# Optimization experiments

Hardware: AMD Instinct MI355X
Metric: run time of the kernel (lower is better)

## Reference

```python
import jax, jax.numpy as jnp
import numpy as np

N_NODES = 100000
N_EDGES = 1200000
F_IN, HID, LAT = 128, 64, 32
N_GRAPHS = 512
NEG_SLOPE = 0.2  # PyG GATConv default


def setup_inputs() -> dict:
    key = jax.random.key(0)
    ks = jax.random.split(key, 20)
    inp = {
        'x': jax.random.normal(ks[0], (N_NODES, F_IN), jnp.float32),
        'edge_index': jax.random.randint(ks[1], (2, N_EDGES), 0, N_NODES, jnp.int32),
        'batch': jnp.sort(jax.random.randint(ks[2], (N_NODES,), 0, N_GRAPHS, jnp.int32)),
    }
    # GAT layer params: W [in,out], a_src/a_dst [out], bias [out] (heads=1)
    dims = [(F_IN, HID), (HID, HID), (HID, HID)]
    for i, (din, dout) in enumerate(dims):
        s = 1.0 / np.sqrt(din)
        inp[f'W{i}'] = jax.random.uniform(ks[3 + 4 * i], (din, dout), jnp.float32, -s, s)
        inp[f'a_src{i}'] = jax.random.normal(ks[4 + 4 * i], (dout,), jnp.float32) * 0.1
        inp[f'a_dst{i}'] = jax.random.normal(ks[5 + 4 * i], (dout,), jnp.float32) * 0.1
        inp[f'b{i}'] = jnp.zeros((dout,), jnp.float32)
    s = 1.0 / np.sqrt(HID)
    inp['fc_W'] = jax.random.uniform(ks[15], (HID, LAT), jnp.float32, -s, s)
    inp['fc_b'] = jnp.zeros((LAT,), jnp.float32)
    return inp


def _gat_layer(x, src, dst, W, a_src, a_dst, b, n):
    h = x @ W                                   # [N, out]
    e = (h @ a_src)[src] + (h @ a_dst)[dst]     # [E+N] raw scores
    e = jnp.where(e > 0, e, NEG_SLOPE * e)      # LeakyReLU
    # segmented softmax over incoming edges of each dst (self-loops guarantee non-empty)
    m = jax.ops.segment_max(e, dst, num_segments=n)
    w = jnp.exp(e - m[dst])
    denom = jax.ops.segment_sum(w, dst, num_segments=n)
    alpha = w / denom[dst]
    out = jax.ops.segment_sum(h[src] * alpha[:, None], dst, num_segments=n)
    return out + b


def reference(x, edge_index, batch, W0, a_src0, a_dst0, b0, W1, a_src1, a_dst1, b1,
              W2, a_src2, a_dst2, b2, fc_W, fc_b):
    n = x.shape[0]
    loops = jnp.arange(n, dtype=edge_index.dtype)
    src = jnp.concatenate([edge_index[0], loops])  # add_self_loops=True
    dst = jnp.concatenate([edge_index[1], loops])
    for (W, a_s, a_d, b) in ((W0, a_src0, a_dst0, b0),
                             (W1, a_src1, a_dst1, b1),
                             (W2, a_src2, a_dst2, b2)):
        x = jax.nn.relu(_gat_layer(x, src, dst, W, a_s, a_d, b, n))
    # dropout is identity in eval mode
    sums = jax.ops.segment_sum(x, batch, num_segments=N_GRAPHS)
    cnt = jax.ops.segment_sum(jnp.ones((n,), x.dtype), batch, num_segments=N_GRAPHS)
    pooled = sums / jnp.maximum(cnt, 1.0)[:, None]  # global_mean_pool
    return pooled @ fc_W + fc_b
```

## Files before the change

### kernel.cpp

```cpp
#include <hip/hip_runtime.h>
#include <hip/hip_bf16.h>
#include <hip/hip_fp16.h>

#define NN 100000
#define NE 1200000
#define NG 512
#define NBK ((NN + 511) / 512)
#define CAP 8192
#define SBATCH 4096
#define EPB (SBATCH / 256)
#define SA_BLOCKS ((NE + SBATCH - 1) / SBATCH)
#define TILES ((NN + 63) / 64)

__global__ void k_binitF(int* gcur) {
    int b = blockIdx.x * blockDim.x + threadIdx.x;
    if (b < NBK) gcur[b] = b * CAP;
}

__device__ __forceinline__ void sortA_body(
    const int* __restrict__ srcA, const int* __restrict__ dstA, int e,
    int* gcur, uint2* __restrict__ ebuf, int bid, int* smemInt) {
    int* cnt = smemInt;
    int* base = smemInt + NBK;
    const int t = threadIdx.x;
    const int i0 = bid * SBATCH;
    for (int b = t; b < NBK; b += 256) cnt[b] = 0;
    __syncthreads();
#pragma unroll
    for (int k = 0; k < EPB; ++k) {
        int i = i0 + k * 256 + t;
        if (i < e) atomicAdd(&cnt[dstA[i] >> 9], 1);
    }
    __syncthreads();
    for (int b = t; b < NBK; b += 256) {
        int c = cnt[b];
        base[b] = c ? atomicAdd(&gcur[b], c) : 0;
        cnt[b] = 0;
    }
    __syncthreads();
#pragma unroll
    for (int k = 0; k < EPB; ++k) {
        int i = i0 + k * 256 + t;
        if (i < e) {
            int d = dstA[i], s = srcA[i];
            int b = d >> 9;
            int off = atomicAdd(&cnt[b], 1);
            int slot = base[b] + off;
            if (slot < (b + 1) * CAP)
                ebuf[slot] = make_uint2((unsigned)s, (unsigned)d);
        }
    }
}

__global__ __launch_bounds__(256) void k_hist2(
    const uint2* __restrict__ ebuf, const int* __restrict__ gcur,
    int* __restrict__ cnt, int n) {
    __shared__ int c512[512];
    const int b = blockIdx.x;
    const int d0 = b << 9;
    const int hi = min(n - d0, 512);
    for (int j = threadIdx.x; j < 512; j += 256) c512[j] = 0;
    __syncthreads();
    const int beg = b * CAP, end = gcur[b];
    for (int i = beg + threadIdx.x; i < end; i += 256)
        atomicAdd(&c512[(int)ebuf[i].y - d0], 1);
    __syncthreads();
    for (int j = threadIdx.x; j < hi; j += 256) cnt[d0 + j] = c512[j] + 1;
}

__global__ void k_scan1(const int* __restrict__ cnt, int n, int* ex, int* blkSum) {
    __shared__ int s[1024];
    int i = blockIdx.x * 1024 + threadIdx.x;
    int v = (i < n) ? cnt[i] : 0;
    s[threadIdx.x] = v;
    __syncthreads();
    for (int off = 1; off < 1024; off <<= 1) {
        int t = (threadIdx.x >= off) ? s[threadIdx.x - off] : 0;
        __syncthreads();
        s[threadIdx.x] += t;
        __syncthreads();
    }
    if (i < n) ex[i] = s[threadIdx.x] - v;
    if (threadIdx.x == 1023) blkSum[blockIdx.x] = s[1023];
}

__global__ void k_scan2(const int* __restrict__ blkSum, int nb, int* blkOff, int* totalOut) {
    __shared__ int s[128];
    int t = threadIdx.x;
    int v = (t < nb) ? blkSum[t] : 0;
    s[t] = v;
    __syncthreads();
    for (int off = 1; off < 128; off <<= 1) {
        int x = (t >= off) ? s[t - off] : 0;
        __syncthreads();
        s[t] += x;
        __syncthreads();
    }
    if (t < nb) blkOff[t] = s[t] - v;
    if (t == 127) *totalOut = s[127];
}

__global__ void k_scan3(int* row_ptr, const int* __restrict__ blkOff, int n) {
    int i = blockIdx.x * blockDim.x + threadIdx.x;
    if (i < n) row_ptr[i] += blkOff[i >> 10];
}

__global__ __launch_bounds__(512) void k_sortB2(
    const uint2* __restrict__ ebuf, const int* __restrict__ gcur,
    const int* __restrict__ row_ptr, int n, int* __restrict__ col) {
    __shared__ int cur[512];
    const int b = blockIdx.x;
    const int d0 = b << 9;
    const int hi = min(n - d0, 512);
    for (int j = threadIdx.x; j < hi; j += 512) {
        int rp = row_ptr[d0 + j];
        col[rp] = d0 + j;
        cur[j] = rp + 1;
    }
    __syncthreads();
    const int beg = b * CAP, end = gcur[b];
    for (int i = beg + threadIdx.x; i < end; i += 512) {
        uint2 r = ebuf[i];
        int pos = atomicAdd(&cur[(int)r.y - d0], 1);
        col[pos] = (int)r.x;
    }
}

#define XP 36
#define WP 68
#define SMEM_FLOATS (64 * XP + 32 * WP)

template <int K, bool HIN>
__device__ __forceinline__ void gemm_body(
    const float* __restrict__ Xf, const __half* __restrict__ Xh,
    const float* __restrict__ W,
    const float* __restrict__ a_src, const float* __restrict__ a_dst,
    __half* __restrict__ H, float* __restrict__ ssrc, float* __restrict__ sdst,
    int n, int tile, float* __restrict__ Xs, float* __restrict__ Ws) {
    constexpr int KC = 32;
    constexpr int NC = K / KC;
    const int tid = threadIdx.x;
    const int row0 = tile * 64;
    const int tx = tid & 15, ty = tid >> 4;
    float acc[4][4] = {};

    for (int c = 0; c < NC; ++c) {
        if (c) __syncthreads();
        for (int i = tid; i < KC * 16; i += 256) {
            int k = i >> 4, c4 = i & 15;
            float4 v = reinterpret_cast<const float4*>(W + (size_t)(c * KC + k) * 64)[c4];
            *reinterpret_cast<float4*>(&Ws[k * WP + c4 * 4]) = v;
        }
        for (int i = tid; i < 64 * 8; i += 256) {
            int r = i >> 3, c4 = i & 7;
            int row = row0 + r;
            float4 v = make_float4(0.f, 0.f, 0.f, 0.f);
            if (row < n) {
                if constexpr (HIN) {
                    float2 raw = reinterpret_cast<const float2*>(Xh + (size_t)row * K + c * KC)[c4];
                    const __half2* ph = reinterpret_cast<const __half2*>(&raw);
                    float2 lo = __half22float2(ph[0]), hi = __half22float2(ph[1]);
                    v = make_float4(lo.x, lo.y, hi.x, hi.y);
                } else {
                    v = reinterpret_cast<const float4*>(Xf + (size_t)row * K + c * KC)[c4];
                }
            }
            *reinterpret_cast<float4*>(&Xs[r * XP + c4 * 4]) = v;
        }
        __syncthreads();

        for (int k = 0; k < KC; k += 4) {
            float4 xv[4], wv[4];
#pragma unroll
            for (int r = 0; r < 4; ++r)
                xv[r] = *reinterpret_cast<const float4*>(&Xs[(ty * 4 + r) * XP + k]);
#pragma unroll
            for (int j = 0; j < 4; ++j)
                wv[j] = *reinterpret_cast<const float4*>(&Ws[(k + j) * WP + tx * 4]);
#pragma unroll
            for (int r = 0; r < 4; ++r) {
                const float* xp = reinterpret_cast<const float*>(&xv[r]);
#pragma unroll
                for (int j = 0; j < 4; ++j) {
                    const float* wp = reinterpret_cast<const float*>(&wv[j]);
#pragma unroll
                    for (int cc = 0; cc < 4; ++cc) acc[r][cc] += xp[j] * wp[cc];
                }
            }
        }
    }

    float4 av = reinterpret_cast<const float4*>(a_src)[tx];
    float4 dv = reinterpret_cast<const float4*>(a_dst)[tx];
#pragma unroll
    for (int r = 0; r < 4; ++r) {
        int row = row0 + ty * 4 + r;
        if (row < n) {
            float2 packed;
            *reinterpret_cast<__half2*>(&packed.x) = __floats2half2_rn(acc[r][0], acc[r][1]);
            *reinterpret_cast<__half2*>(&packed.y) = __floats2half2_rn(acc[r][2], acc[r][3]);
            reinterpret_cast<float2*>(H + (size_t)row * 64)[tx] = packed;
            float ps = acc[r][0] * av.x + acc[r][1] * av.y + acc[r][2] * av.z + acc[r][3] * av.w;
            float pd = acc[r][0] * dv.x + acc[r][1] * dv.y + acc[r][2] * dv.z + acc[r][3] * dv.w;
#pragma unroll
            for (int off = 1; off < 16; off <<= 1) {
                ps += __shfl_xor(ps, off);
                pd += __shfl_xor(pd, off);
            }
            if (tx == 0) {
                ssrc[row] = ps;
                sdst[row] = pd;
            }
        }
    }
}

__global__ __launch_bounds__(256) void k_g0sA(
    const int* __restrict__ srcA, const int* __restrict__ dstA,
    int* gcur, uint2* __restrict__ ebuf,
    const float* __restrict__ Xf, const float* __restrict__ W,
    const float* __restrict__ a_src, const float* __restrict__ a_dst,
    __half* __restrict__ H, float* __restrict__ ssrc, float* __restrict__ sdst, int n) {
    __shared__ float smem[SMEM_FLOATS];
    if (blockIdx.x < TILES) {
        gemm_body<128, false>(Xf, nullptr, W, a_src, a_dst, H, ssrc, sdst, n,
                              blockIdx.x, smem, smem + 64 * XP);
    } else {
        sortA_body(srcA, dstA, NE, gcur, ebuf, blockIdx.x - TILES,
                   reinterpret_cast<int*>(smem));
    }
}

template <int K, bool HIN>
__global__ __launch_bounds__(256) void k_gemm_att(
    const float* __restrict__ Xf, const __half* __restrict__ Xh,
    const float* __restrict__ W,
    const float* __restrict__ a_src, const float* __restrict__ a_dst,
    __half* __restrict__ H, float* __restrict__ ssrc, float* __restrict__ sdst, int n) {
    __shared__ float smem[SMEM_FLOATS];
    gemm_body<K, HIN>(Xf, Xh, W, a_src, a_dst, H, ssrc, sdst, n,
                      blockIdx.x, smem, smem + 64 * XP);
}

__global__ __launch_bounds__(256) void k_agg5(
    const float2* __restrict__ H2, const float* __restrict__ ssrc,
    const float* __restrict__ sdst, const int* __restrict__ row_ptr,
    const int* __restrict__ col, const float4* __restrict__ bias4,
    float2* __restrict__ Yh2, int n) {
    const int wave = threadIdx.x >> 6, lane = threadIdx.x & 63;
    const int hf = lane >> 5, hl = lane & 31;
    const int base = blockIdx.x * 8 + wave * 2;
    const int dst = base + hf;

    int beg = 0, end = 0;
    if (dst < n) { beg = row_ptr[dst]; end = row_ptr[dst + 1]; }
    int deg = end - beg;
    int dmax = max(deg, __shfl_xor(deg, 32));

    if (dmax <= 32) {
        float sd = (dst < n) ? sdst[dst] : 0.f;
        int s_l = 0;
        float e = -INFINITY;
        if (hl < deg) {
            s_l = col[beg + hl];
            e = ssrc[s_l] + sd;
            e = (e > 0.f) ? e : 0.2f * e;
        }
        float m = e;
#pragma unroll
        for (int off = 16; off; off >>= 1) m = fmaxf(m, __shfl_xor(m, off));
        float w_l = (hl < deg) ? __expf(e - m) : 0.f;
        float den = w_l;
#pragma unroll
        for (int off = 16; off; off >>= 1) den += __shfl_xor(den, off);

        const int grp = hl >> 4, fl = hl & 15;
        float4 acc = make_float4(0.f, 0.f, 0.f, 0.f);
        for (int jj = 0; jj < deg; jj += 8) {
            int j0 = jj + grp, j1 = jj + 2 + grp, j2 = jj + 4 + grp, j3 = jj + 6 + grp;
            int s0 = __shfl(s_l, hf * 32 + j0), s1 = __shfl(s_l, hf * 32 + j1);
            int s2 = __shfl(s_l, hf * 32 + j2), s3 = __shfl(s_l, hf * 32 + j3);
            float w0 = __shfl(w_l, hf * 32 + j0), w1 = __shfl(w_l, hf * 32 + j1);
            float w2 = __shfl(w_l, hf * 32 + j2), w3 = __shfl(w_l, hf * 32 + j3);
            if (j0 < deg) {
                float2 raw = H2[(size_t)s0 * 16 + fl];
                const __half2* ph = reinterpret_cast<const __half2*>(&raw);
                float2 lo = __half22float2(ph[0]), hi = __half22float2(ph[1]);
                acc.x += w0 * lo.x; acc.y += w0 * lo.y;
                acc.z += w0 * hi.x; acc.w += w0 * hi.y;
            }
            if (j1 < deg) {
                float2 raw = H2[(size_t)s1 * 16 + fl];
                const __half2* ph = reinterpret_cast<const __half2*>(&raw);
                float2 lo = __half22float2(ph[0]), hi = __half22float2(ph[1]);
                acc.x += w1 * lo.x; acc.y += w1 * lo.y;
                acc.z += w1 * hi.x; acc.w += w1 * hi.y;
            }
            if (j2 < deg) {
                float2 raw = H2[(size_t)s2 * 16 + fl];
                const __half2* ph = reinterpret_cast<const __half2*>(&raw);
                float2 lo = __half22float2(ph[0]), hi = __half22float2(ph[1]);
                acc.x += w2 * lo.x; acc.y += w2 * lo.y;
                acc.z += w2 * hi.x; acc.w += w2 * hi.y;
            }
            if (j3 < deg) {
                float2 raw = H2[(size_t)s3 * 16 + fl];
                const __half2* ph = reinterpret_cast<const __half2*>(&raw);
                float2 lo = __half22float2(ph[0]), hi = __half22float2(ph[1]);
                acc.x += w3 * lo.x; acc.y += w3 * lo.y;
                acc.z += w3 * hi.x; acc.w += w3 * hi.y;
            }
        }
        acc.x += __shfl_xor(acc.x, 16);
        acc.y += __shfl_xor(acc.y, 16);
        acc.z += __shfl_xor(acc.z, 16);
        acc.w += __shfl_xor(acc.w, 16);
        if (grp == 0 && dst < n) {
            float inv = 1.f / den;
            float4 b = bias4[fl];
            float ox = fmaxf(acc.x * inv + b.x, 0.f);
            float oy = fmaxf(acc.y * inv + b.y, 0.f);
            float oz = fmaxf(acc.z * inv + b.z, 0.f);
            float ow = fmaxf(acc.w * inv + b.w, 0.f);
            float2 packed;
            *reinterpret_cast<__half2*>(&packed.x) = __floats2half2_rn(ox, oy);
            *reinterpret_cast<__half2*>(&packed.y) = __floats2half2_rn(oz, ow);
            Yh2[(size_t)dst * 16 + fl] = packed;
        }
    } else {
        for (int h = 0; h < 2; ++h) {
            int d = base + h;
            if (d >= n) break;
            int bg = row_ptr[d], en = row_ptr[d + 1];
            float sdd = sdst[d];
            float m = -INFINITY, d2 = 0.f;
            for (int c = bg; c < en; c += 64) {
                int j = c + lane;
                float e = -INFINITY;
                if (j < en) {
                    e = ssrc[col[j]] + sdd;
                    e = (e > 0.f) ? e : 0.2f * e;
                }
                float cm = e;
#pragma unroll
                for (int off = 32; off; off >>= 1) cm = fmaxf(cm, __shfl_xor(cm, off));
                float nm = fmaxf(m, cm);
                float term = (j < en) ? __expf(e - nm) : 0.f;
#pragma unroll
                for (int off = 32; off; off >>= 1) term += __shfl_xor(term, off);
                d2 = d2 * __expf(m - nm) + term;
                m = nm;
            }
            const int g4 = lane >> 4, fl = lane & 15;
            float4 acc = make_float4(0.f, 0.f, 0.f, 0.f);
            for (int jj = 0; jj < en - bg; jj += 8) {
                int j0 = bg + jj + g4, j1 = bg + jj + 4 + g4;
                if (j0 < en) {
                    int s = col[j0];
                    float e = ssrc[s] + sdd;
                    e = (e > 0.f) ? e : 0.2f * e;
                    float wgt = __expf(e - m);
                    float2 raw = H2[(size_t)s * 16 + fl];
                    const __half2* ph = reinterpret_cast<const __half2*>(&raw);
                    float2 lo = __half22float2(ph[0]), hi = __half22float2(ph[1]);
                    acc.x += wgt * lo.x; acc.y += wgt * lo.y;
                    acc.z += wgt * hi.x; acc.w += wgt * hi.y;
                }
                if (j1 < en) {
                    int s = col[j1];
                    float e = ssrc[s] + sdd;
                    e = (e > 0.f) ? e : 0.2f * e;
                    float wgt = __expf(e - m);
                    float2 raw = H2[(size_t)s * 16 + fl];
                    const __half2* ph = reinterpret_cast<const __half2*>(&raw);
                    float2 lo = __half22float2(ph[0]), hi = __half22float2(ph[1]);
                    acc.x += wgt * lo.x; acc.y += wgt * lo.y;
                    acc.z += wgt * hi.x; acc.w += wgt * hi.y;
                }
            }
#pragma unroll
            for (int off = 16; off < 64; off <<= 1) {
                acc.x += __shfl_xor(acc.x, off);
                acc.y += __shfl_xor(acc.y, off);
                acc.z += __shfl_xor(acc.z, off);
                acc.w += __shfl_xor(acc.w, off);
            }
            if (g4 == 0) {
                float inv = 1.f / d2;
                float4 b = bias4[fl];
                float ox = fmaxf(acc.x * inv + b.x, 0.f);
                float oy = fmaxf(acc.y * inv + b.y, 0.f);
                float oz = fmaxf(acc.z * inv + b.z, 0.f);
                float ow = fmaxf(acc.w * inv + b.w, 0.f);
                float2 packed;
                *reinterpret_cast<__half2*>(&packed.x) = __floats2half2_rn(ox, oy);
                *reinterpret_cast<__half2*>(&packed.y) = __floats2half2_rn(oz, ow);
                Yh2[(size_t)d * 16 + fl] = packed;
            }
        }
    }
}

__global__ void k_gstart(const int* __restrict__ batch, int n, int* gs) {
    int g = blockIdx.x * blockDim.x + threadIdx.x;
    if (g > NG) return;
    int lo = 0, hi = n;
    while (lo < hi) {
        int mid = (lo + hi) >> 1;
        if (batch[mid] < g) lo = mid + 1; else hi = mid;
    }
    gs[g] = lo;
}

__global__ __launch_bounds__(256) void k_pool_fc(
    const float2* __restrict__ Yh2, const int* __restrict__ gs,
    const float* __restrict__ fcW, const float* __restrict__ fcb,
    float* __restrict__ out) {
    __shared__ float4 part[4][16];
    __shared__ float p[64];
    const int g = blockIdx.x, tid = threadIdx.x;
    const int wave = tid >> 6, lane = tid & 63;
    const int grp = lane >> 4, fl = lane & 15;
    const int b = gs[g], e = gs[g + 1];

    float4 acc = make_float4(0.f, 0.f, 0.f, 0.f);
    for (int r = b + wave * 4 + grp; r < e; r += 16) {
        float2 raw = Yh2[(size_t)r * 16 + fl];
        const __half2* ph = reinterpret_cast<const __half2*>(&raw);
        float2 lo = __half22float2(ph[0]), hi = __half22float2(ph[1]);
        acc.x += lo.x; acc.y += lo.y; acc.z += hi.x; acc.w += hi.y;
    }
#pragma unroll
    for (int off = 16; off < 64; off <<= 1) {
        acc.x += __shfl_xor(acc.x, off);
        acc.y += __shfl_xor(acc.y, off);
        acc.z += __shfl_xor(acc.z, off);
        acc.w += __shfl_xor(acc.w, off);
    }
    if (grp == 0) part[wave][fl] = acc;
    __syncthreads();
    if (tid < 16) {
        float4 s0 = part[0][tid], s1 = part[1][tid], s2 = part[2][tid], s3 = part[3][tid];
        float inv = 1.f / (float)((e - b) > 0 ? (e - b) : 1);
        p[tid * 4 + 0] = (s0.x + s1.x + s2.x + s3.x) * inv;
        p[tid * 4 + 1] = (s0.y + s1.y + s2.y + s3.y) * inv;
        p[tid * 4 + 2] = (s0.z + s1.z + s2.z + s3.z) * inv;
        p[tid * 4 + 3] = (s0.w + s1.w + s2.w + s3.w) * inv;
    }
    __syncthreads();
    if (tid < 32) {
        float accO = fcb[tid];
#pragma unroll
        for (int k = 0; k < 64; ++k) accO += p[k] * fcW[k * 32 + tid];
        out[g * 32 + tid] = accO;
    }
}

extern "C" void kernel_launch(void* const* d_in, const int* in_sizes, int n_in,
                              void* d_out, int out_size, void* d_ws, size_t ws_size,
                              hipStream_t stream) {
    const float* x = (const float*)d_in[0];
    const int* ei = (const int*)d_in[1];
    const int* batch = (const int*)d_in[2];
    const float* W0 = (const float*)d_in[3];
    const float* as0 = (const float*)d_in[4];
    const float* ad0 = (const float*)d_in[5];
    const float* b0 = (const float*)d_in[6];
    const float* W1 = (const float*)d_in[7];
    const float* as1 = (const float*)d_in[8];
    const float* ad1 = (const float*)d_in[9];
    const float* b1 = (const float*)d_in[10];
    const float* W2 = (const float*)d_in[11];
    const float* as2 = (const float*)d_in[12];
    const float* ad2 = (const float*)d_in[13];
    const float* b2 = (const float*)d_in[14];
    const float* fcW = (const float*)d_in[15];
    const float* fcb = (const float*)d_in[16];
    float* out = (float*)d_out;

    char* w = (char*)d_ws;
    auto alloc = [&](size_t bytes) {
        void* p = (void*)w;
        w += (bytes + 255) & ~(size_t)255;
        return p;
    };
    int* cnt = (int*)alloc((size_t)NN * 4);
    int* row_ptr = (int*)alloc((size_t)(NN + 1) * 4);
    int* blkSum = (int*)alloc(512);
    int* blkOff = (int*)alloc(512);
    int* gcur = (int*)alloc((size_t)NBK * 4);
    int* col = (int*)alloc((size_t)(NE + NN) * 4);
    int* gs = (int*)alloc((size_t)(NG + 1) * 4);
    uint2* ebuf = (uint2*)alloc((size_t)NBK * CAP * 8);
    __half* Ha = (__half*)alloc((size_t)NN * 64 * 2);
    __half* Hb = (__half*)alloc((size_t)NN * 64 * 2);
    __half* Y = (__half*)alloc((size_t)NN * 64 * 2);
    float* ssA = (float*)alloc((size_t)NN * 4);
    float* sdA = (float*)alloc((size_t)NN * 4);
    float* ssB = (float*)alloc((size_t)NN * 4);
    float* sdB = (float*)alloc((size_t)NN * 4);

    const int* srcA = ei;
    const int* dstA = ei + NE;

    k_binitF<<<1, 256, 0, stream>>>(gcur);
    k_g0sA<<<TILES + SA_BLOCKS, 256, 0, stream>>>(srcA, dstA, gcur, ebuf,
                                                  x, W0, as0, ad0, Ha, ssA, sdA, NN);
    k_hist2<<<NBK, 256, 0, stream>>>(ebuf, gcur, cnt, NN);
    const int nb = (NN + 1023) / 1024;
    k_scan1<<<nb, 1024, 0, stream>>>(cnt, NN, row_ptr, blkSum);
    k_scan2<<<1, 128, 0, stream>>>(blkSum, nb, blkOff, row_ptr + NN);
    k_scan3<<<(NN + 255) / 256, 256, 0, stream>>>(row_ptr, blkOff, NN);
    k_sortB2<<<NBK, 512, 0, stream>>>(ebuf, gcur, row_ptr, NN, col);
    k_gstart<<<3, 256, 0, stream>>>(batch, NN, gs);

    const int agg_grid = (NN + 7) / 8;

    k_agg5<<<agg_grid, 256, 0, stream>>>((const float2*)Ha, ssA, sdA, row_ptr, col,
                                         (const float4*)b0, (float2*)Hb, NN);
    k_gemm_att<64, true><<<TILES, 256, 0, stream>>>(nullptr, Hb, W1, as1, ad1,
                                                    Ha, ssB, sdB, NN);
    k_agg5<<<agg_grid, 256, 0, stream>>>((const float2*)Ha, ssB, sdB, row_ptr, col,
                                         (const float4*)b1, (float2*)Hb, NN);
    k_gemm_att<64, true><<<TILES, 256, 0, stream>>>(nullptr, Hb, W2, as2, ad2,
                                                    Ha, ssA, sdA, NN);
    k_agg5<<<agg_grid, 256, 0, stream>>>((const float2*)Ha, ssA, sdA, row_ptr, col,
                                         (const float4*)b2, (float2*)Y, NN);

    k_pool_fc<<<NG, 256, 0, stream>>>((const float2*)Y, gs, fcW, fcb, out);
}
```

Measured before the change: 248.1 us.

## Replace histogram plus three-pass scan with bucket-level prefix and in-block placement

The per-node histogram and three-kernel global scan are replaced by a single small kernel that scans per-bucket edge counts and computes the graph starts, followed by one kernel per bucket that histograms, scans locally, writes row_ptr and places edges. This cuts the CSR build from six launches to two and drops the cnt/blkSum round trips through global memory. The placement kernel now reads ebuf twice within one block. The fused first kernel also runs the sort blocks ahead of the GEMM tiles.

```diff
diff --git a/kernel.cpp b/kernel.cpp
--- a/kernel.cpp
+++ b/kernel.cpp
@@ -52,76 +52,77 @@
     }
 }
 
-__global__ __launch_bounds__(256) void k_hist2(
+__global__ __launch_bounds__(256) void k_bucketPfx(
+    const int* __restrict__ gcur, int* __restrict__ bstart, int* __restrict__ row_ptr,
+    const int* __restrict__ batch, int* __restrict__ gs, int n) {
+    if (blockIdx.x == 0) {
+        __shared__ int s[256];
+        const int t = threadIdx.x;
+        int v = 0;
+        if (t < NBK) {
+            int d0 = t << 9;
+            int hi = min(n - d0, 512);
+            int edges = min(gcur[t] - t * CAP, CAP);
+            v = edges + hi;
+        }
+        s[t] = v;
+        __syncthreads();
+        for (int off = 1; off < 256; off <<= 1) {
+            int x = (t >= off) ? s[t - off] : 0;
+            __syncthreads();
+            s[t] += x;
+            __syncthreads();
+        }
+        if (t < NBK) bstart[t] = s[t] - v;
+        if (t == NBK - 1) row_ptr[n] = s[t];
+    } else {
+        int g = (blockIdx.x - 1) * 256 + threadIdx.x;
+        if (g > NG) return;
+        int lo = 0, hi = n;
+        while (lo < hi) {
+            int mid = (lo + hi) >> 1;
+            if (batch[mid] < g) lo = mid + 1; else hi = mid;
+        }
+        gs[g] = lo;
+    }
+}
+
+__global__ __launch_bounds__(512) void k_place(
     const uint2* __restrict__ ebuf, const int* __restrict__ gcur,
-    int* __restrict__ cnt, int n) {
-    __shared__ int c512[512];
+    const int* __restrict__ bstart, int* __restrict__ row_ptr,
+    int* __restrict__ col, int n) {
+    __shared__ int cnt[512];
+    __shared__ int scn[512];
     const int b = blockIdx.x;
     const int d0 = b << 9;
     const int hi = min(n - d0, 512);
-    for (int j = threadIdx.x; j < 512; j += 256) c512[j] = 0;
-    __syncthreads();
-    const int beg = b * CAP, end = gcur[b];
-    for (int i = beg + threadIdx.x; i < end; i += 256)
-        atomicAdd(&c512[(int)ebuf[i].y - d0], 1);
-    __syncthreads();
-    for (int j = threadIdx.x; j < hi; j += 256) cnt[d0 + j] = c512[j] + 1;
-}
-
-__global__ void k_scan1(const int* __restrict__ cnt, int n, int* ex, int* blkSum) {
-    __shared__ int s[1024];
-    int i = blockIdx.x * 1024 + threadIdx.x;
-    int v = (i < n) ? cnt[i] : 0;
-    s[threadIdx.x] = v;
-    __syncthreads();
-    for (int off = 1; off < 1024; off <<= 1) {
-        int t = (threadIdx.x >= off) ? s[threadIdx.x - off] : 0;
+    const int t = threadIdx.x;
+    cnt[t] = (t < hi) ? 1 : 0;
+    __syncthreads();
+    const int beg = b * CAP;
+    const int end = min(gcur[b], beg + CAP);
+    for (int i = beg + t; i < end; i += 512)
+        atomicAdd(&cnt[(int)ebuf[i].y - d0], 1);
+    __syncthreads();
+    int v = cnt[t];
+    scn[t] = v;
+    __syncthreads();
+    for (int off = 1; off < 512; off <<= 1) {
+        int x = (t >= off) ? scn[t - off] : 0;
         __syncthreads();
-        s[threadIdx.x] += t;
+        scn[t] += x;
         __syncthreads();
     }
-    if (i < n) ex[i] = s[threadIdx.x] - v;
-    if (threadIdx.x == 1023) blkSum[blockIdx.x] = s[1023];
-}
-
-__global__ void k_scan2(const int* __restrict__ blkSum, int nb, int* blkOff, int* totalOut) {
-    __shared__ int s[128];
-    int t = threadIdx.x;
-    int v = (t < nb) ? blkSum[t] : 0;
-    s[t] = v;
-    __syncthreads();
-    for (int off = 1; off < 128; off <<= 1) {
-        int x = (t >= off) ? s[t - off] : 0;
-        __syncthreads();
-        s[t] += x;
-        __syncthreads();
-    }
-    if (t < nb) blkOff[t] = s[t] - v;
-    if (t == 127) *totalOut = s[127];
-}
-
-__global__ void k_scan3(int* row_ptr, const int* __restrict__ blkOff, int n) {
-    int i = blockIdx.x * blockDim.x + threadIdx.x;
-    if (i < n) row_ptr[i] += blkOff[i >> 10];
-}
-
-__global__ __launch_bounds__(512) void k_sortB2(
-    const uint2* __restrict__ ebuf, const int* __restrict__ gcur,
-    const int* __restrict__ row_ptr, int n, int* __restrict__ col) {
-    __shared__ int cur[512];
-    const int b = blockIdx.x;
-    const int d0 = b << 9;
-    const int hi = min(n - d0, 512);
-    for (int j = threadIdx.x; j < hi; j += 512) {
-        int rp = row_ptr[d0 + j];
-        col[rp] = d0 + j;
-        cur[j] = rp + 1;
-    }
-    __syncthreads();
-    const int beg = b * CAP, end = gcur[b];
-    for (int i = beg + threadIdx.x; i < end; i += 512) {
+    int rp = bstart[b] + scn[t] - v;
+    if (t < hi) {
+        row_ptr[d0 + t] = rp;
+        col[rp] = d0 + t;
+        cnt[t] = rp + 1;
+    }
+    __syncthreads();
+    for (int i = beg + t; i < end; i += 512) {
         uint2 r = ebuf[i];
-        int pos = atomicAdd(&cur[(int)r.y - d0], 1);
+        int pos = atomicAdd(&cnt[(int)r.y - d0], 1);
         col[pos] = (int)r.x;
     }
 }
@@ -222,12 +223,11 @@
     const float* __restrict__ a_src, const float* __restrict__ a_dst,
     __half* __restrict__ H, float* __restrict__ ssrc, float* __restrict__ sdst, int n) {
     __shared__ float smem[SMEM_FLOATS];
-    if (blockIdx.x < TILES) {
+    if (blockIdx.x < SA_BLOCKS) {
+        sortA_body(srcA, dstA, NE, gcur, ebuf, blockIdx.x, reinterpret_cast<int*>(smem));
+    } else {
         gemm_body<128, false>(Xf, nullptr, W, a_src, a_dst, H, ssrc, sdst, n,
-                              blockIdx.x, smem, smem + 64 * XP);
-    } else {
-        sortA_body(srcA, dstA, NE, gcur, ebuf, blockIdx.x - TILES,
-                   reinterpret_cast<int*>(smem));
+                              blockIdx.x - SA_BLOCKS, smem, smem + 64 * XP);
     }
 }
 
@@ -401,17 +401,6 @@
     }
 }
 
-__global__ void k_gstart(const int* __restrict__ batch, int n, int* gs) {
-    int g = blockIdx.x * blockDim.x + threadIdx.x;
-    if (g > NG) return;
-    int lo = 0, hi = n;
-    while (lo < hi) {
-        int mid = (lo + hi) >> 1;
-        if (batch[mid] < g) lo = mid + 1; else hi = mid;
-    }
-    gs[g] = lo;
-}
-
 __global__ __launch_bounds__(256) void k_pool_fc(
     const float2* __restrict__ Yh2, const int* __restrict__ gs,
     const float* __restrict__ fcW, const float* __restrict__ fcb,
@@ -484,10 +473,8 @@
         w += (bytes + 255) & ~(size_t)255;
         return p;
     };
-    int* cnt = (int*)alloc((size_t)NN * 4);
     int* row_ptr = (int*)alloc((size_t)(NN + 1) * 4);
-    int* blkSum = (int*)alloc(512);
-    int* blkOff = (int*)alloc(512);
+    int* bstart = (int*)alloc((size_t)NBK * 4);
     int* gcur = (int*)alloc((size_t)NBK * 4);
     int* col = (int*)alloc((size_t)(NE + NN) * 4);
     int* gs = (int*)alloc((size_t)(NG + 1) * 4);
@@ -504,15 +491,10 @@
     const int* dstA = ei + NE;
 
     k_binitF<<<1, 256, 0, stream>>>(gcur);
-    k_g0sA<<<TILES + SA_BLOCKS, 256, 0, stream>>>(srcA, dstA, gcur, ebuf,
+    k_g0sA<<<SA_BLOCKS + TILES, 256, 0, stream>>>(srcA, dstA, gcur, ebuf,
                                                   x, W0, as0, ad0, Ha, ssA, sdA, NN);
-    k_hist2<<<NBK, 256, 0, stream>>>(ebuf, gcur, cnt, NN);
-    const int nb = (NN + 1023) / 1024;
-    k_scan1<<<nb, 1024, 0, stream>>>(cnt, NN, row_ptr, blkSum);
-    k_scan2<<<1, 128, 0, stream>>>(blkSum, nb, blkOff, row_ptr + NN);
-    k_scan3<<<(NN + 255) / 256, 256, 0, stream>>>(row_ptr, blkOff, NN);
-    k_sortB2<<<NBK, 512, 0, stream>>>(ebuf, gcur, row_ptr, NN, col);
-    k_gstart<<<3, 256, 0, stream>>>(batch, NN, gs);
+    k_bucketPfx<<<4, 256, 0, stream>>>(gcur, bstart, row_ptr, batch, gs, NN);
+    k_place<<<NBK, 512, 0, stream>>>(ebuf, gcur, bstart, row_ptr, col, NN);
 
     const int agg_grid = (NN + 7) / 8;
 
```

New measurement: 234.6 us. 1.06x faster.
